# Performance work log

Hardware: AMD Instinct MI355X
Metric: run time of the kernel (lower is better)

The kernel has to match this reference:

```python
import jax, jax.numpy as jnp
import numpy as np

H = 16  # num_heads

def setup_inputs() -> dict:
    key = jax.random.key(0)
    ks = jax.random.split(key, 5)
    B, L, D = 2, 2048, 1024
    x = jax.random.normal(ks[0], (B, L, D), dtype=jnp.float32)
    # causal mask: masked_fill where mask == 0
    attn_mask = jnp.tril(jnp.ones((L, L), dtype=jnp.int32))
    scale = 1.0 / np.sqrt(D)
    Wq = jax.random.normal(ks[1], (D, D), dtype=jnp.float32) * scale
    Wk = jax.random.normal(ks[2], (D, D), dtype=jnp.float32) * scale
    Wv = jax.random.normal(ks[3], (D, D), dtype=jnp.float32) * scale
    Wo = jax.random.normal(ks[4], (D, D), dtype=jnp.float32) * scale
    return {"x": x, "attn_mask": attn_mask, "Wq": Wq, "Wk": Wk, "Wv": Wv, "Wo": Wo}

def reference(x, attn_mask, Wq, Wk, Wv, Wo):
    B, L, D = x.shape
    dh = D // H
    # nn.Linear with no bias: y = x @ W^T
    q = (x @ Wq.T).reshape(B, L, H, dh)
    k = (x @ Wk.T).reshape(B, L, H, dh)
    v = (x @ Wv.T).reshape(B, L, H, dh)
    # scores: [B, H, L, L]
    scores = jnp.einsum('blhd,bmhd->bhlm', q, k) / jnp.sqrt(jnp.array(dh, x.dtype))
    scores = jnp.where(attn_mask == 0, -jnp.inf, scores)
    attn = jax.nn.softmax(scores, axis=-1)
    out = jnp.einsum('bhlm,bmhd->blhd', attn, v).reshape(B, L, D)
    return out @ Wo.T
```

## Files before the change

kernel.cpp:

```cpp
#include <hip/hip_runtime.h>
#include <math.h>

#define L_SEQ  2048
#define D_MODEL 1024
#define N_HEAD 16
#define D_HEAD 64
#define B_SIZE 2

typedef __attribute__((ext_vector_type(8))) short bf16x8;
typedef __attribute__((ext_vector_type(4))) float f32x4;
typedef unsigned short u16;
typedef unsigned int u32;

__device__ __forceinline__ f32x4 mfma16(bf16x8 a, bf16x8 b, f32x4 c) {
    return __builtin_amdgcn_mfma_f32_16x16x32_bf16(a, b, c, 0, 0, 0);
}

__device__ __forceinline__ u16 f2bf(float x) {
    u32 u = __builtin_bit_cast(u32, x);
    u32 r = (u + 0x7FFFu + ((u >> 16) & 1u)) >> 16;
    return (u16)r;
}
__device__ __forceinline__ u16 f2bf_t(float x) {
    return (u16)(__builtin_bit_cast(u32, x) >> 16);
}
__device__ __forceinline__ float bf2f(u16 h) {
    u32 u = ((u32)h) << 16;
    return __builtin_bit_cast(float, u);
}

__device__ __forceinline__ void gl2lds16(const void* g, void* l) {
    __builtin_amdgcn_global_load_lds(
        (__attribute__((address_space(1))) void*)(g),
        (__attribute__((address_space(3))) void*)(l), 16, 0, 0);
}

__global__ __launch_bounds__(256) void split_hl(const float* __restrict__ in,
                                                u16* __restrict__ out) {
    const int idx = blockIdx.x * 256 + threadIdx.x;
    const int c4 = idx << 2;
    const int r = c4 >> 10, c = c4 & 1023;
    float4 v = *(const float4*)(in + c4);
    u16 h0 = f2bf(v.x), h1 = f2bf(v.y), h2 = f2bf(v.z), h3 = f2bf(v.w);
    ushort4 hi = make_ushort4(h0, h1, h2, h3);
    ushort4 lo = make_ushort4(f2bf(v.x - bf2f(h0)), f2bf(v.y - bf2f(h1)),
                              f2bf(v.z - bf2f(h2)), f2bf(v.w - bf2f(h3)));
    *(ushort4*)(out + (size_t)r * 2048 + c) = hi;
    *(ushort4*)(out + (size_t)r * 2048 + 1024 + c) = lo;
}

__global__ __launch_bounds__(256) void split_w4(
    const float* __restrict__ w0, const float* __restrict__ w1,
    const float* __restrict__ w2, const float* __restrict__ w3,
    u16* __restrict__ outbase) {
    const float* in = (blockIdx.y == 0) ? w0 : (blockIdx.y == 1) ? w1
                      : (blockIdx.y == 2) ? w2 : w3;
    u16* out = outbase + (size_t)blockIdx.y * 2097152;
    const int idx = blockIdx.x * 256 + threadIdx.x;
    const int c4 = idx << 2;
    const int r = c4 >> 10, c = c4 & 1023;
    float4 v = *(const float4*)(in + c4);
    u16 h0 = f2bf(v.x), h1 = f2bf(v.y), h2 = f2bf(v.z), h3 = f2bf(v.w);
    ushort4 hi = make_ushort4(h0, h1, h2, h3);
    ushort4 lo = make_ushort4(f2bf(v.x - bf2f(h0)), f2bf(v.y - bf2f(h1)),
                              f2bf(v.z - bf2f(h2)), f2bf(v.w - bf2f(h3)));
    *(ushort4*)(out + (size_t)r * 2048 + c) = hi;
    *(ushort4*)(out + (size_t)r * 2048 + 1024 + c) = lo;
}

__device__ __forceinline__ int kaOf(int x) {
    return (((x >> 4) == 1) ? 1024 : 0) + ((x << 6) & 1023);
}
__device__ __forceinline__ int kwOf(int x) {
    return (((x >> 4) == 0) ? 1024 : 0) + ((x << 6) & 1023);
}

#define SBAR()  do { __builtin_amdgcn_sched_barrier(0); \
                     __builtin_amdgcn_s_barrier(); \
                     __builtin_amdgcn_sched_barrier(0); } while (0)

__global__ __launch_bounds__(512) void gemm256_qkv(
    const u16* __restrict__ A2, const u16* __restrict__ Wall,
    u16* __restrict__ Qh, u16* __restrict__ Ql,
    u16* __restrict__ Kh, u16* __restrict__ Kl,
    u16* __restrict__ Vh) {
    extern __shared__ __align__(16) u16 smem[];

    const int t = threadIdx.x, l = t & 63, wid = t >> 6;
    const int id = blockIdx.x;
    const int wg = (id & 7) * 24 + (id >> 3);
    const int mt = wg / 12, ntile = wg % 12;
    const int m0 = mt << 8, n0 = ntile << 8;

    const int wrH = wid >> 2;
    const int wc = (wid & 3) << 6;
    const int bHalf = (wid & 3) >> 1;
    const int brB = (wid & 1) << 6;

    f32x4 acc[8][4];
#pragma unroll
    for (int i = 0; i < 8; ++i)
#pragma unroll
        for (int j = 0; j < 4; ++j) acc[i][j] = (f32x4){0.f, 0.f, 0.f, 0.f};

    const int sr = t >> 3, sc = t & 7;

    auto stageA = [&](int x, int half) {
        const int koff = kaOf(x);
        u16* dst = smem + ((x & 1) * 32768) + half * 8192;
        const u16* srcb = A2 + (size_t)(m0 + half * 128) * 2048 + koff;
#pragma unroll
        for (int p = 0; p < 2; ++p) {
            const int r = sr + p * 64;
            const int ck = sc ^ (r & 7);
            gl2lds16(srcb + (size_t)r * 2048 + ck * 8, dst + (t + p * 512) * 8);
        }
    };
    auto stageB = [&](int x, int half) {
        const int koff = kwOf(x);
        u16* dst = smem + 16384 + ((x & 1) * 32768) + half * 8192;
        const u16* srcb = Wall + (size_t)(n0 + half * 128) * 2048 + koff;
#pragma unroll
        for (int p = 0; p < 2; ++p) {
            const int r = sr + p * 64;
            const int ck = sc ^ (r & 7);
            gl2lds16(srcb + (size_t)r * 2048 + ck * 8, dst + (t + p * 512) * 8);
        }
    };
    auto dsA = [&](int s, int mh, int kc, bf16x8 af[4]) {
        const u16* Ab = smem + s * 32768 + wrH * 8192;
#pragma unroll
        for (int f = 0; f < 4; ++f) {
            const int r = mh * 64 + f * 16 + (l & 15);
            const int c8 = kc * 4 + (l >> 4);
            af[f] = *(const bf16x8*)&Ab[r * 64 + ((c8 ^ (r & 7)) << 3)];
        }
    };
    auto dsB = [&](int s, int kc, bf16x8 bfr[4]) {
        const u16* Bb = smem + 16384 + s * 32768 + bHalf * 8192;
#pragma unroll
        for (int f = 0; f < 4; ++f) {
            const int r = brB + f * 16 + (l & 15);
            const int c8 = kc * 4 + (l >> 4);
            bfr[f] = *(const bf16x8*)&Bb[r * 64 + ((c8 ^ (r & 7)) << 3)];
        }
    };

    stageB(0, 0); stageB(0, 1); stageA(0, 0); stageA(0, 1);
    stageB(1, 0); stageB(1, 1);
    __builtin_amdgcn_sched_barrier(0);
    asm volatile("s_waitcnt vmcnt(4)" ::: "memory");
    __builtin_amdgcn_s_barrier();
    __builtin_amdgcn_sched_barrier(0);

    const int NT = 48;
    bf16x8 breg0[4], breg1[4], af[4];
    for (int tt = 0; tt < NT; ++tt) {
        const int s = tt & 1;
        dsA(s, 0, 0, af); dsB(s, 0, breg0);
        if (tt + 1 < NT) stageA(tt + 1, 0);
        SBAR();
        __builtin_amdgcn_s_setprio(1);
#pragma unroll
        for (int f = 0; f < 4; ++f)
#pragma unroll
            for (int fn = 0; fn < 4; ++fn)
                acc[f][fn] = mfma16(af[f], breg0[fn], acc[f][fn]);
        __builtin_amdgcn_s_setprio(0);
        SBAR();
        dsA(s, 0, 1, af); dsB(s, 1, breg1);
        if (tt + 1 < NT) stageA(tt + 1, 1);
        SBAR();
        __builtin_amdgcn_s_setprio(1);
#pragma unroll
        for (int f = 0; f < 4; ++f)
#pragma unroll
            for (int fn = 0; fn < 4; ++fn)
                acc[f][fn] = mfma16(af[f], breg1[fn], acc[f][fn]);
        __builtin_amdgcn_s_setprio(0);
        SBAR();
        dsA(s, 1, 0, af);
        if (tt + 2 < NT) stageB(tt + 2, 0);
        SBAR();
        __builtin_amdgcn_s_setprio(1);
#pragma unroll
        for (int f = 0; f < 4; ++f)
#pragma unroll
            for (int fn = 0; fn < 4; ++fn)
                acc[4 + f][fn] = mfma16(af[f], breg0[fn], acc[4 + f][fn]);
        __builtin_amdgcn_s_setprio(0);
        SBAR();
        dsA(s, 1, 1, af);
        if (tt + 2 < NT) stageB(tt + 2, 1);
        SBAR();
        __builtin_amdgcn_s_setprio(1);
#pragma unroll
        for (int f = 0; f < 4; ++f)
#pragma unroll
            for (int fn = 0; fn < 4; ++fn)
                acc[4 + f][fn] = mfma16(af[f], breg1[fn], acc[4 + f][fn]);
        __builtin_amdgcn_s_setprio(0);
        __builtin_amdgcn_sched_barrier(0);
        if (tt + 2 < NT) {
            asm volatile("s_waitcnt vmcnt(4)" ::: "memory");
        } else if (tt + 1 < NT) {
            asm volatile("s_waitcnt vmcnt(0)" ::: "memory");
        }
        __builtin_amdgcn_s_barrier();
        __builtin_amdgcn_sched_barrier(0);
    }

#pragma unroll
    for (int fm = 0; fm < 8; ++fm)
#pragma unroll
        for (int fn = 0; fn < 4; ++fn)
#pragma unroll
            for (int rg = 0; rg < 4; ++rg) {
                const int gm = m0 + wrH * 128 + fm * 16 + ((l >> 4) << 2) + rg;
                const int gn = n0 + wc + fn * 16 + (l & 15);
                const int z = gn >> 10, col = gn & 1023;
                float v = acc[fm][fn][rg];
                if (z == 0) v *= 0.125f;
                const int b = gm >> 11, lq = gm & 2047;
                const int h = col >> 6, d = col & 63;
                const size_t oi = (((size_t)(b * 16 + h)) * 2048 + lq) * 64 + d;
                const u16 hi = f2bf(v);
                if (z == 0) { Qh[oi] = hi; Ql[oi] = f2bf(v - bf2f(hi)); }
                else if (z == 1) { Kh[oi] = hi; Kl[oi] = f2bf(v - bf2f(hi)); }
                else { Vh[oi] = hi; }
            }
}

template <int MODE>
__global__ __launch_bounds__(256) void gemm_ks(
    const u16* __restrict__ A2, const u16* __restrict__ Wbase,
    float* __restrict__ Cout) {
    __shared__ __align__(16) u16 As[128 * 32];
    __shared__ __align__(16) u16 Ws[128 * 32];
    const int t = threadIdx.x, l = t & 63, wid = t >> 6;
    const int m0 = blockIdx.y << 7, n0 = blockIdx.x << 7;
    const u16* W2 = Wbase;

    f32x4 acc[4][4];
#pragma unroll
    for (int i = 0; i < 4; ++i)
#pragma unroll
        for (int j = 0; j < 4; ++j) acc[i][j] = (f32x4){0.f, 0.f, 0.f, 0.f};

    int orow[2], ocs[2];
#pragma unroll
    for (int p = 0; p < 2; ++p) {
        int o = wid * 1024 + l * 16 + p * 4096;
        orow[p] = o >> 6;
        ocs[p] = ((o >> 4) & 3) ^ ((o >> 6) & 3);
    }
    const int wr = (wid >> 1) << 6, wc = (wid & 1) << 6;

    for (int k0 = 0; k0 < 3072; k0 += 32) {
        const int rg3 = k0 >> 10, kb = k0 & 1023;
        const int ka = (rg3 == 1 ? 1024 : 0) + kb;
        const int kw = (rg3 == 0 ? 1024 : 0) + kb;
        __syncthreads();
#pragma unroll
        for (int p = 0; p < 2; ++p) {
            gl2lds16(A2 + (size_t)(m0 + orow[p]) * 2048 + ka + ocs[p] * 8,
                     (u16*)As + (wid * 512 + p * 2048));
            gl2lds16(W2 + (size_t)(n0 + orow[p]) * 2048 + kw + ocs[p] * 8,
                     (u16*)Ws + (wid * 512 + p * 2048));
        }
        __syncthreads();
        bf16x8 af[4], bfr[4];
#pragma unroll
        for (int f = 0; f < 4; ++f) {
            int row = wr + (f << 4) + (l & 15);
            int ch = (l >> 4) ^ (row & 3);
            af[f] = *(const bf16x8*)&As[(row << 5) + (ch << 3)];
            int rown = wc + (f << 4) + (l & 15);
            int chn = (l >> 4) ^ (rown & 3);
            bfr[f] = *(const bf16x8*)&Ws[(rown << 5) + (chn << 3)];
        }
#pragma unroll
        for (int fm = 0; fm < 4; ++fm)
#pragma unroll
            for (int fn = 0; fn < 4; ++fn)
                acc[fm][fn] = mfma16(af[fm], bfr[fn], acc[fm][fn]);
    }

#pragma unroll
    for (int fm = 0; fm < 4; ++fm)
#pragma unroll
        for (int fn = 0; fn < 4; ++fn)
#pragma unroll
            for (int rg = 0; rg < 4; ++rg) {
                int gm = m0 + wr + (fm << 4) + ((l >> 4) << 2) + rg;
                int gn = n0 + wc + (fn << 4) + (l & 15);
                Cout[(size_t)gm * 1024 + gn] = acc[fm][fn][rg];
            }
}

__global__ __launch_bounds__(128) void vtrans(const u16* __restrict__ Vh,
                                              u16* __restrict__ Vth) {
    const int t = threadIdx.x;
    const int kt = (blockIdx.x << 1) + (t >> 6);
    const int h = blockIdx.y, b = blockIdx.z;
    const size_t base = ((size_t)(b * 16 + h)) * 131072;
    const int kv0 = kt << 6;
    const int st = t & 63;
    const int r0 = (st >> 3) << 3;
    const int c0 = (st & 7) << 3;
    ushort4 inv[8][2];
#pragma unroll
    for (int j = 0; j < 8; ++j) {
        const u16* p = Vh + base + (size_t)(kv0 + r0 + j) * 64 + c0;
        inv[j][0] = *(const ushort4*)p;
        inv[j][1] = *(const ushort4*)(p + 4);
    }
#pragma unroll
    for (int i = 0; i < 8; ++i) {
        u16 o[8];
#pragma unroll
        for (int j = 0; j < 8; ++j) {
            ushort4 vv = inv[j][i >> 2];
            const int ii = i & 3;
            o[j] = (ii == 0) ? vv.x : (ii == 1) ? vv.y : (ii == 2) ? vv.z : vv.w;
        }
        u16* q = Vth + base + (size_t)(c0 + i) * 2048 + kv0 + r0;
        *(ushort4*)q = make_ushort4(o[0], o[1], o[2], o[3]);
        *(ushort4*)(q + 4) = make_ushort4(o[4], o[5], o[6], o[7]);
    }
}

struct QTileState {
    bf16x8 qhf[2], qlf[2];
    f32x4 oacc[4];
    float mrow[4], lrow[4];
};

__device__ __forceinline__ void qstate_init(
    QTileState& st, const u16* Qh, const u16* Ql, size_t hb, int q0, int w, int l) {
    const int rowq = q0 + (w << 4) + (l & 15);
#pragma unroll
    for (int kc = 0; kc < 2; ++kc) {
        const size_t off = hb + (size_t)rowq * 64 + (((kc << 2) + (l >> 4)) << 3);
        st.qhf[kc] = *(const bf16x8*)(Qh + off);
        st.qlf[kc] = *(const bf16x8*)(Ql + off);
    }
#pragma unroll
    for (int i = 0; i < 4; ++i) {
        st.oacc[i] = (f32x4){0.f, 0.f, 0.f, 0.f};
        st.mrow[i] = -INFINITY;
        st.lrow[i] = 0.f;
    }
}

__device__ __forceinline__ void fa_compute(
    QTileState& st, const u16* bKh, const u16* bKl,
    const u16* bVh, int kv0, int q0, int w, int l, u16* Pw) {
    if (kv0 > q0 + (w << 4) + 15) return;

    f32x4 sacc[4];
#pragma unroll
    for (int nf = 0; nf < 4; ++nf) sacc[nf] = (f32x4){0.f, 0.f, 0.f, 0.f};
#pragma unroll
    for (int kc = 0; kc < 2; ++kc) {
        bf16x8 kh_[4], kl_[4];
#pragma unroll
        for (int nf = 0; nf < 4; ++nf) {
            const int row = (nf << 4) + (l & 15);
            const int ch = ((kc << 2) + (l >> 4)) ^ (row & 7);
            kh_[nf] = *(const bf16x8*)&bKh[(row << 6) + (ch << 3)];
            kl_[nf] = *(const bf16x8*)&bKl[(row << 6) + (ch << 3)];
        }
        __builtin_amdgcn_s_setprio(1);
#pragma unroll
        for (int nf = 0; nf < 4; ++nf) {
            sacc[nf] = mfma16(st.qhf[kc], kl_[nf], sacc[nf]);
            sacc[nf] = mfma16(st.qlf[kc], kh_[nf], sacc[nf]);
            sacc[nf] = mfma16(st.qhf[kc], kh_[nf], sacc[nf]);
        }
        __builtin_amdgcn_s_setprio(0);
    }

    const bool domask = (kv0 + 63) > (q0 + (w << 4));
    float pm[4] = {-INFINITY, -INFINITY, -INFINITY, -INFINITY};
    float sv[4][4];
#pragma unroll
    for (int nf = 0; nf < 4; ++nf)
#pragma unroll
        for (int rg = 0; rg < 4; ++rg) {
            float x = sacc[nf][rg];
            if (domask) {
                const int colg = kv0 + (nf << 4) + (l & 15);
                const int rowg = q0 + (w << 4) + ((l >> 4) << 2) + rg;
                if (colg > rowg) x = -INFINITY;
            }
            sv[nf][rg] = x;
            pm[rg] = fmaxf(pm[rg], x);
        }
#pragma unroll
    for (int rg = 0; rg < 4; ++rg) {
        float v = pm[rg];
        v = fmaxf(v, __shfl_xor(v, 1));
        v = fmaxf(v, __shfl_xor(v, 2));
        v = fmaxf(v, __shfl_xor(v, 4));
        v = fmaxf(v, __shfl_xor(v, 8));
        pm[rg] = v;
    }
    const float need = fmaxf(fmaxf(pm[0] - st.mrow[0], pm[1] - st.mrow[1]),
                             fmaxf(pm[2] - st.mrow[2], pm[3] - st.mrow[3]));
    if (__any(need > 8.0f)) {
#pragma unroll
        for (int rg = 0; rg < 4; ++rg) {
            const float mn = fmaxf(st.mrow[rg], pm[rg]);
            const float al = __expf(st.mrow[rg] - mn);
            st.mrow[rg] = mn;
            st.lrow[rg] *= al;
#pragma unroll
            for (int nf = 0; nf < 4; ++nf) st.oacc[nf][rg] *= al;
        }
    }
    float ps[4] = {0.f, 0.f, 0.f, 0.f};
    u16 pb[4][4];
#pragma unroll
    for (int nf = 0; nf < 4; ++nf)
#pragma unroll
        for (int rg = 0; rg < 4; ++rg) {
            const float p = __expf(sv[nf][rg] - st.mrow[rg]);
            ps[rg] += p;
            pb[nf][rg] = f2bf_t(p);
        }
#pragma unroll
    for (int rg = 0; rg < 4; ++rg) {
        float v = ps[rg];
        v += __shfl_xor(v, 1);
        v += __shfl_xor(v, 2);
        v += __shfl_xor(v, 4);
        v += __shfl_xor(v, 8);
        st.lrow[rg] += v;
    }

#pragma unroll
    for (int nf = 0; nf < 4; ++nf)
#pragma unroll
        for (int rg = 0; rg < 4; ++rg) {
            const int r = ((l >> 4) << 2) + rg;
            const int c = (nf << 4) + (l & 15);
            const int ch = (c >> 3) ^ (r & 7);
            Pw[(r << 6) + (ch << 3) + (c & 7)] = pb[nf][rg];
        }
#pragma unroll
    for (int kc = 0; kc < 2; ++kc) {
        const int r = l & 15;
        const int chp = ((kc << 2) + (l >> 4)) ^ (r & 7);
        const bf16x8 pa = *(const bf16x8*)&Pw[(r << 6) + (chp << 3)];
        bf16x8 vh_[4];
#pragma unroll
        for (int nf = 0; nf < 4; ++nf) {
            const int row = (nf << 4) + (l & 15);
            const int cv = ((kc << 2) + (l >> 4)) ^ (row & 7);
            vh_[nf] = *(const bf16x8*)&bVh[(row << 6) + (cv << 3)];
        }
        __builtin_amdgcn_s_setprio(1);
#pragma unroll
        for (int nf = 0; nf < 4; ++nf)
            st.oacc[nf] = mfma16(pa, vh_[nf], st.oacc[nf]);
        __builtin_amdgcn_s_setprio(0);
    }
}

__device__ __forceinline__ void fa_epilogue(
    QTileState& st, u16* A2, int g, int q0, int w, int l) {
    const int b = g >> 4, h = g & 15;
    float inv[4];
#pragma unroll
    for (int rg = 0; rg < 4; ++rg) inv[rg] = 1.0f / st.lrow[rg];
#pragma unroll
    for (int nf = 0; nf < 4; ++nf)
#pragma unroll
        for (int rg = 0; rg < 4; ++rg) {
            const int rowq = q0 + (w << 4) + ((l >> 4) << 2) + rg;
            const int m = (b << 11) + rowq;
            const int d = (nf << 4) + (l & 15);
            const float v = st.oacc[nf][rg] * inv[rg];
            const u16 hi = f2bf(v);
            const u16 lo = f2bf(v - bf2f(hi));
            const size_t rb = (size_t)m * 2048;
            A2[rb + h * 64 + d] = hi;
            A2[rb + 1024 + h * 64 + d] = lo;
        }
}

__global__ __launch_bounds__(512) void flash_mfma(
    const u16* __restrict__ Qh, const u16* __restrict__ Ql,
    const u16* __restrict__ Kh, const u16* __restrict__ Kl,
    const u16* __restrict__ Vth,
    u16* __restrict__ A2) {
    extern __shared__ __align__(16) u16 smem[];
    u16* const KhsA = smem;
    u16* const KlsA = smem + 4096;
    u16* const VhsA = smem + 8192;
    u16* const KhsB = smem + 12288;
    u16* const KlsB = smem + 16384;
    u16* const VhsB = smem + 20480;
    u16* const Ps   = smem + 24576;

    const int t = threadIdx.x, l = t & 63, w = t >> 6;
    const int id = blockIdx.x;
    const int nid = ((id & 7) << 5) + (id >> 3);
    const int g = nid >> 3;
    const int p = nid & 7;
    const int q0A = p << 7;
    const int q0B = (15 - p) << 7;
    const size_t hb = (size_t)g * 131072;

    QTileState stA, stB;
    qstate_init(stA, Qh, Ql, hb, q0A, w, l);
    qstate_init(stB, Qh, Ql, hb, q0B, w, l);

    const int row_s = t >> 3;
    const int cs_s = (t & 7) ^ (row_s & 7);

    auto stage = [&](u16* dKh, u16* dKl, u16* dVh, int kt_) {
        const int kv0s = kt_ << 6;
        const size_t koff = hb + (size_t)(kv0s + row_s) * 64 + cs_s * 8;
        gl2lds16(Kh + koff, dKh + t * 8);
        gl2lds16(Kl + koff, dKl + t * 8);
        const size_t voff = hb + (size_t)row_s * 2048 + kv0s + cs_s * 8;
        gl2lds16(Vth + voff, dVh + t * 8);
    };

    u16* const Pw = Ps + (w << 10);
    const int ntA = (p << 1) + 2;
    const int ntB = 32 - (p << 1);

    stage(KhsA, KlsA, VhsA, 0);
    __syncthreads();
    for (int kt = 0; kt < ntB; kt += 2) {
        stage(KhsB, KlsB, VhsB, kt + 1);
        fa_compute(stB, KhsA, KlsA, VhsA, kt << 6, q0B, w, l, Pw);
        if (kt < ntA)
            fa_compute(stA, KhsA, KlsA, VhsA, kt << 6, q0A, w, l, Pw);
        __syncthreads();
        if (kt + 2 < ntB) stage(KhsA, KlsA, VhsA, kt + 2);
        fa_compute(stB, KhsB, KlsB, VhsB, (kt + 1) << 6, q0B, w, l, Pw);
        if (kt + 1 < ntA)
            fa_compute(stA, KhsB, KlsB, VhsB, (kt + 1) << 6, q0A, w, l, Pw);
        __syncthreads();
    }

    fa_epilogue(stA, A2, g, q0A, w, l);
    fa_epilogue(stB, A2, g, q0B, w, l);
}

__global__ __launch_bounds__(256) void gemm_bt_f32(
    const float* __restrict__ A, const float* __restrict__ W,
    float* __restrict__ C, int M, int N, int K) {
    __shared__ float As[16][68];
    __shared__ float Bs[16][68];
    const int t = threadIdx.x;
    const int tx = t & 15, ty = t >> 4;
    const int m0 = blockIdx.y << 6, n0 = blockIdx.x << 6;
    const int lr = t >> 2, lc = (t & 3) << 2;
    const float* Ag = A + (size_t)(m0 + lr) * K + lc;
    const float* Wg = W + (size_t)(n0 + lr) * K + lc;
    float acc[4][4];
#pragma unroll
    for (int i = 0; i < 4; ++i)
#pragma unroll
        for (int j = 0; j < 4; ++j) acc[i][j] = 0.f;
    for (int k0 = 0; k0 < K; k0 += 16) {
        const float4 av = *(const float4*)(Ag + k0);
        const float4 wv = *(const float4*)(Wg + k0);
        __syncthreads();
        As[lc + 0][lr] = av.x; As[lc + 1][lr] = av.y;
        As[lc + 2][lr] = av.z; As[lc + 3][lr] = av.w;
        Bs[lc + 0][lr] = wv.x; Bs[lc + 1][lr] = wv.y;
        Bs[lc + 2][lr] = wv.z; Bs[lc + 3][lr] = wv.w;
        __syncthreads();
#pragma unroll
        for (int kk = 0; kk < 16; ++kk) {
            const float4 a = *(const float4*)&As[kk][ty << 2];
            const float4 b = *(const float4*)&Bs[kk][tx << 2];
            acc[0][0] += a.x * b.x; acc[0][1] += a.x * b.y; acc[0][2] += a.x * b.z; acc[0][3] += a.x * b.w;
            acc[1][0] += a.y * b.x; acc[1][1] += a.y * b.y; acc[1][2] += a.y * b.z; acc[1][3] += a.y * b.w;
            acc[2][0] += a.z * b.x; acc[2][1] += a.z * b.y; acc[2][2] += a.z * b.z; acc[2][3] += a.z * b.w;
            acc[3][0] += a.w * b.x; acc[3][1] += a.w * b.y; acc[3][2] += a.w * b.z; acc[3][3] += a.w * b.w;
        }
    }
#pragma unroll
    for (int i = 0; i < 4; ++i) {
        float4 o;
        o.x = acc[i][0]; o.y = acc[i][1]; o.z = acc[i][2]; o.w = acc[i][3];
        *(float4*)&C[(size_t)(m0 + (ty << 2) + i) * N + n0 + (tx << 2)] = o;
    }
}

#define SW(row, seg) ((((seg) ^ (((row) + ((row) >> 4)) & 15)) << 2))

__global__ __launch_bounds__(256) void flash_f32(
    const float* __restrict__ Q, const float* __restrict__ K,
    const float* __restrict__ V, float* __restrict__ O) {
    __shared__ float Qs[64 * 64];
    __shared__ float KPs[64 * 64];
    __shared__ float Vs[64 * 64];
    const int t = threadIdx.x;
    const int tx = t & 15, ty = t >> 4;
    const int qt = blockIdx.x, h = blockIdx.y, b = blockIdx.z;
    const int q0 = qt << 6;
    const size_t hbase = (size_t)b * L_SEQ * D_MODEL + (size_t)h * D_HEAD;
#pragma unroll
    for (int i = 0; i < 4; ++i) {
        const int idx = t + (i << 8);
        const int rr = idx >> 4, seg = idx & 15;
        const float4 qv = *(const float4*)&Q[hbase + (size_t)(q0 + rr) * D_MODEL + (seg << 2)];
        *(float4*)&Qs[rr * 64 + SW(rr, seg)] = qv;
    }
    float m[4], lr_[4], oacc[4][4];
#pragma unroll
    for (int i = 0; i < 4; ++i) {
        m[i] = -INFINITY; lr_[i] = 0.f;
#pragma unroll
        for (int j = 0; j < 4; ++j) oacc[i][j] = 0.f;
    }
    const int ntile = qt + 1;
    for (int kt = 0; kt < ntile; ++kt) {
        const int kv0 = kt << 6;
        __syncthreads();
#pragma unroll
        for (int i = 0; i < 4; ++i) {
            const int idx = t + (i << 8);
            const int rr = idx >> 4, seg = idx & 15;
            const float4 kv = *(const float4*)&K[hbase + (size_t)(kv0 + rr) * D_MODEL + (seg << 2)];
            const float4 vv = *(const float4*)&V[hbase + (size_t)(kv0 + rr) * D_MODEL + (seg << 2)];
            *(float4*)&KPs[rr * 64 + SW(rr, seg)] = kv;
            *(float4*)&Vs[rr * 64 + SW(rr, seg)] = vv;
        }
        __syncthreads();
        float s[4][4];
#pragma unroll
        for (int i = 0; i < 4; ++i)
#pragma unroll
            for (int j = 0; j < 4; ++j) s[i][j] = 0.f;
#pragma unroll
        for (int seg = 0; seg < 16; ++seg) {
            float4 qv[4], kv[4];
#pragma unroll
            for (int i = 0; i < 4; ++i) {
                const int R = (ty << 2) + i;
                qv[i] = *(const float4*)&Qs[R * 64 + SW(R, seg)];
            }
#pragma unroll
            for (int j = 0; j < 4; ++j) {
                const int Cc = (tx << 2) + j;
                kv[j] = *(const float4*)&KPs[Cc * 64 + SW(Cc, seg)];
            }
#pragma unroll
            for (int i = 0; i < 4; ++i)
#pragma unroll
                for (int j = 0; j < 4; ++j)
                    s[i][j] += qv[i].x * kv[j].x + qv[i].y * kv[j].y +
                               qv[i].z * kv[j].z + qv[i].w * kv[j].w;
        }
        const bool diag = (kt == qt);
        float tm[4];
#pragma unroll
        for (int i = 0; i < 4; ++i) {
            tm[i] = -INFINITY;
#pragma unroll
            for (int j = 0; j < 4; ++j) {
                float sval = s[i][j] * 0.125f;
                if (diag) {
                    const int Cg = kv0 + (tx << 2) + j;
                    const int Rg = q0 + (ty << 2) + i;
                    if (Cg > Rg) sval = -INFINITY;
                }
                s[i][j] = sval;
                tm[i] = fmaxf(tm[i], sval);
            }
            tm[i] = fmaxf(tm[i], __shfl_xor(tm[i], 1));
            tm[i] = fmaxf(tm[i], __shfl_xor(tm[i], 2));
            tm[i] = fmaxf(tm[i], __shfl_xor(tm[i], 4));
            tm[i] = fmaxf(tm[i], __shfl_xor(tm[i], 8));
        }
        float p[4][4];
#pragma unroll
        for (int i = 0; i < 4; ++i) {
            const float mn = fmaxf(m[i], tm[i]);
            const float alpha = __expf(m[i] - mn);
            m[i] = mn;
            float psum = 0.f;
#pragma unroll
            for (int j = 0; j < 4; ++j) {
                p[i][j] = __expf(s[i][j] - mn);
                psum += p[i][j];
            }
            psum += __shfl_xor(psum, 1);
            psum += __shfl_xor(psum, 2);
            psum += __shfl_xor(psum, 4);
            psum += __shfl_xor(psum, 8);
            lr_[i] = lr_[i] * alpha + psum;
#pragma unroll
            for (int j = 0; j < 4; ++j) oacc[i][j] *= alpha;
        }
        __syncthreads();
#pragma unroll
        for (int i = 0; i < 4; ++i) {
            const int R = (ty << 2) + i;
            float4 pv;
            pv.x = p[i][0]; pv.y = p[i][1]; pv.z = p[i][2]; pv.w = p[i][3];
            *(float4*)&KPs[R * 64 + SW(R, tx)] = pv;
        }
        __syncthreads();
#pragma unroll
        for (int cs = 0; cs < 16; ++cs) {
            float pc[4][4];
            float4 vr[4];
#pragma unroll
            for (int i = 0; i < 4; ++i) {
                const int R = (ty << 2) + i;
                const float4 pr = *(const float4*)&KPs[R * 64 + SW(R, cs)];
                pc[i][0] = pr.x; pc[i][1] = pr.y; pc[i][2] = pr.z; pc[i][3] = pr.w;
            }
#pragma unroll
            for (int cc = 0; cc < 4; ++cc) {
                const int Cr = (cs << 2) + cc;
                vr[cc] = *(const float4*)&Vs[Cr * 64 + SW(Cr, tx)];
            }
#pragma unroll
            for (int i = 0; i < 4; ++i)
#pragma unroll
                for (int cc = 0; cc < 4; ++cc) {
                    oacc[i][0] += pc[i][cc] * vr[cc].x;
                    oacc[i][1] += pc[i][cc] * vr[cc].y;
                    oacc[i][2] += pc[i][cc] * vr[cc].z;
                    oacc[i][3] += pc[i][cc] * vr[cc].w;
                }
        }
    }
#pragma unroll
    for (int i = 0; i < 4; ++i) {
        const int R = (ty << 2) + i;
        const float invl = 1.0f / lr_[i];
        float4 o;
        o.x = oacc[i][0] * invl; o.y = oacc[i][1] * invl;
        o.z = oacc[i][2] * invl; o.w = oacc[i][3] * invl;
        *(float4*)&O[hbase + (size_t)(q0 + R) * D_MODEL + (tx << 2)] = o;
    }
}

extern "C" void kernel_launch(void* const* d_in, const int* in_sizes, int n_in,
                              void* d_out, int out_size, void* d_ws, size_t ws_size,
                              hipStream_t stream) {
    const float* x  = (const float*)d_in[0];
    const float* Wq = (const float*)d_in[2];
    const float* Wk = (const float*)d_in[3];
    const float* Wv = (const float*)d_in[4];
    const float* Wo = (const float*)d_in[5];
    float* out = (float*)d_out;

    if (ws_size >= 83886080ull) {
        char* ws = (char*)d_ws;
        u16* x2  = (u16*)(ws);
        u16* Wq2 = (u16*)(ws + 16777216);
        u16* Wo2 = (u16*)(ws + 29360128);
        u16* Qh  = (u16*)(ws + 33554432);
        u16* Ql  = (u16*)(ws + 41943040);
        u16* Kh  = (u16*)(ws + 50331648);
        u16* Kl  = (u16*)(ws + 58720256);
        u16* Vth = (u16*)(ws + 67108864);
        u16* Vh  = (u16*)d_out;

        hipFuncSetAttribute((const void*)flash_mfma,
                            hipFuncAttributeMaxDynamicSharedMemorySize, 65536);
        hipFuncSetAttribute((const void*)gemm256_qkv,
                            hipFuncAttributeMaxDynamicSharedMemorySize, 131072);

        split_hl<<<4096, 256, 0, stream>>>(x, x2);
        split_w4<<<dim3(1024, 4), 256, 0, stream>>>(Wq, Wk, Wv, Wo, Wq2);
        gemm256_qkv<<<192, 512, 131072, stream>>>(x2, Wq2, Qh, Ql, Kh, Kl, Vh);
        vtrans<<<dim3(16, 16, 2), 128, 0, stream>>>(Vh, Vth);
        flash_mfma<<<256, 512, 65536, stream>>>(Qh, Ql, Kh, Kl, Vth, x2);
        gemm_ks<0><<<dim3(8, 32), 256, 0, stream>>>(x2, Wo2, out);
    } else {
        const int M = B_SIZE * L_SEQ, N = D_MODEL, Kd = D_MODEL;
        float* Qw = (float*)d_ws;
        float* Kw = Qw + (size_t)M * D_MODEL;
        float* Vw = Kw + (size_t)M * D_MODEL;
        float* Aw = Vw + (size_t)M * D_MODEL;
        dim3 gg(N / 64, M / 64);
        gemm_bt_f32<<<gg, 256, 0, stream>>>(x, Wq, Qw, M, N, Kd);
        gemm_bt_f32<<<gg, 256, 0, stream>>>(x, Wk, Kw, M, N, Kd);
        gemm_bt_f32<<<gg, 256, 0, stream>>>(x, Wv, Vw, M, N, Kd);
        flash_f32<<<dim3(L_SEQ / 64, N_HEAD, B_SIZE), 256, 0, stream>>>(Qw, Kw, Vw, Aw);
        gemm_bt_f32<<<gg, 256, 0, stream>>>(Aw, Wo, out, M, N, Kd);
    }
}
```

Baseline: 250.8 us.

## Interleave two query tiles per KV unit, retile output GEMM, merge split kernels

```diff
diff --git a/kernel.cpp b/kernel.cpp
--- a/kernel.cpp
+++ b/kernel.cpp
@@ -35,28 +35,24 @@
         (__attribute__((address_space(3))) void*)(l), 16, 0, 0);
 }
 
-__global__ __launch_bounds__(256) void split_hl(const float* __restrict__ in,
-                                                u16* __restrict__ out) {
-    const int idx = blockIdx.x * 256 + threadIdx.x;
-    const int c4 = idx << 2;
-    const int r = c4 >> 10, c = c4 & 1023;
-    float4 v = *(const float4*)(in + c4);
-    u16 h0 = f2bf(v.x), h1 = f2bf(v.y), h2 = f2bf(v.z), h3 = f2bf(v.w);
-    ushort4 hi = make_ushort4(h0, h1, h2, h3);
-    ushort4 lo = make_ushort4(f2bf(v.x - bf2f(h0)), f2bf(v.y - bf2f(h1)),
-                              f2bf(v.z - bf2f(h2)), f2bf(v.w - bf2f(h3)));
-    *(ushort4*)(out + (size_t)r * 2048 + c) = hi;
-    *(ushort4*)(out + (size_t)r * 2048 + 1024 + c) = lo;
-}
-
-__global__ __launch_bounds__(256) void split_w4(
+__global__ __launch_bounds__(256) void split_all(
+    const float* __restrict__ x,
     const float* __restrict__ w0, const float* __restrict__ w1,
     const float* __restrict__ w2, const float* __restrict__ w3,
-    u16* __restrict__ outbase) {
-    const float* in = (blockIdx.y == 0) ? w0 : (blockIdx.y == 1) ? w1
-                      : (blockIdx.y == 2) ? w2 : w3;
-    u16* out = outbase + (size_t)blockIdx.y * 2097152;
-    const int idx = blockIdx.x * 256 + threadIdx.x;
+    u16* __restrict__ x2, u16* __restrict__ wout) {
+    const int id = blockIdx.x;
+    const float* in;
+    u16* out;
+    int idx;
+    if (id < 4096) {
+        in = x; out = x2; idx = id * 256 + threadIdx.x;
+    } else {
+        const int wi = (id - 4096) >> 10;
+        const int blk = (id - 4096) & 1023;
+        in = (wi == 0) ? w0 : (wi == 1) ? w1 : (wi == 2) ? w2 : w3;
+        out = wout + (size_t)wi * 2097152;
+        idx = blk * 256 + threadIdx.x;
+    }
     const int c4 = idx << 2;
     const int r = c4 >> 10, c = c4 & 1023;
     float4 v = *(const float4*)(in + c4);
@@ -231,69 +227,71 @@
             }
 }
 
-template <int MODE>
-__global__ __launch_bounds__(256) void gemm_ks(
-    const u16* __restrict__ A2, const u16* __restrict__ Wbase,
+__global__ __launch_bounds__(256) void gemm_wo(
+    const u16* __restrict__ A2, const u16* __restrict__ W2,
     float* __restrict__ Cout) {
     __shared__ __align__(16) u16 As[128 * 32];
-    __shared__ __align__(16) u16 Ws[128 * 32];
+    __shared__ __align__(16) u16 Ws2[64 * 32];
     const int t = threadIdx.x, l = t & 63, wid = t >> 6;
-    const int m0 = blockIdx.y << 7, n0 = blockIdx.x << 7;
-    const u16* W2 = Wbase;
-
-    f32x4 acc[4][4];
+    const int id = blockIdx.x;
+    const int nid = ((id & 7) << 6) + (id >> 3);
+    const int m0 = (nid >> 4) << 7;
+    const int n0 = (nid & 15) << 6;
+    const int wm = wid >> 1, wn = wid & 1;
+
+    f32x4 acc[4][2];
 #pragma unroll
     for (int i = 0; i < 4; ++i)
 #pragma unroll
-        for (int j = 0; j < 4; ++j) acc[i][j] = (f32x4){0.f, 0.f, 0.f, 0.f};
-
-    int orow[2], ocs[2];
-#pragma unroll
-    for (int p = 0; p < 2; ++p) {
-        int o = wid * 1024 + l * 16 + p * 4096;
-        orow[p] = o >> 6;
-        ocs[p] = ((o >> 4) & 3) ^ ((o >> 6) & 3);
-    }
-    const int wr = (wid >> 1) << 6, wc = (wid & 1) << 6;
+        for (int j = 0; j < 2; ++j) acc[i][j] = (f32x4){0.f, 0.f, 0.f, 0.f};
+
+    const int arow0 = t >> 2, ach0 = (t & 3) ^ (arow0 & 3);
+    const int arow1 = (t + 256) >> 2, ach1 = (t & 3) ^ (arow1 & 3);
+    const int brow = t >> 2, bch = (t & 3) ^ (brow & 3);
 
     for (int k0 = 0; k0 < 3072; k0 += 32) {
         const int rg3 = k0 >> 10, kb = k0 & 1023;
         const int ka = (rg3 == 1 ? 1024 : 0) + kb;
         const int kw = (rg3 == 0 ? 1024 : 0) + kb;
         __syncthreads();
-#pragma unroll
-        for (int p = 0; p < 2; ++p) {
-            gl2lds16(A2 + (size_t)(m0 + orow[p]) * 2048 + ka + ocs[p] * 8,
-                     (u16*)As + (wid * 512 + p * 2048));
-            gl2lds16(W2 + (size_t)(n0 + orow[p]) * 2048 + kw + ocs[p] * 8,
-                     (u16*)Ws + (wid * 512 + p * 2048));
-        }
-        __syncthreads();
-        bf16x8 af[4], bfr[4];
+        gl2lds16(A2 + (size_t)(m0 + arow0) * 2048 + ka + ach0 * 8,
+                 (u16*)As + t * 8);
+        gl2lds16(A2 + (size_t)(m0 + arow1) * 2048 + ka + ach1 * 8,
+                 (u16*)As + (t + 256) * 8);
+        if (t < 256)
+            gl2lds16(W2 + (size_t)(n0 + brow) * 2048 + kw + bch * 8,
+                     (u16*)Ws2 + t * 8);
+        __syncthreads();
+        bf16x8 af[4], bfr[2];
 #pragma unroll
         for (int f = 0; f < 4; ++f) {
-            int row = wr + (f << 4) + (l & 15);
-            int ch = (l >> 4) ^ (row & 3);
+            const int row = wm * 64 + f * 16 + (l & 15);
+            const int ch = (l >> 4) ^ (row & 3);
             af[f] = *(const bf16x8*)&As[(row << 5) + (ch << 3)];
-            int rown = wc + (f << 4) + (l & 15);
-            int chn = (l >> 4) ^ (rown & 3);
-            bfr[f] = *(const bf16x8*)&Ws[(rown << 5) + (chn << 3)];
-        }
+        }
+#pragma unroll
+        for (int f = 0; f < 2; ++f) {
+            const int rown = wn * 32 + f * 16 + (l & 15);
+            const int chn = (l >> 4) ^ (rown & 3);
+            bfr[f] = *(const bf16x8*)&Ws2[(rown << 5) + (chn << 3)];
+        }
+        __builtin_amdgcn_s_setprio(1);
 #pragma unroll
         for (int fm = 0; fm < 4; ++fm)
 #pragma unroll
-            for (int fn = 0; fn < 4; ++fn)
+            for (int fn = 0; fn < 2; ++fn)
                 acc[fm][fn] = mfma16(af[fm], bfr[fn], acc[fm][fn]);
+        __builtin_amdgcn_s_setprio(0);
     }
 
 #pragma unroll
     for (int fm = 0; fm < 4; ++fm)
 #pragma unroll
-        for (int fn = 0; fn < 4; ++fn)
+        for (int fn = 0; fn < 2; ++fn)
 #pragma unroll
             for (int rg = 0; rg < 4; ++rg) {
-                int gm = m0 + wr + (fm << 4) + ((l >> 4) << 2) + rg;
-                int gn = n0 + wc + (fn << 4) + (l & 15);
+                const int gm = m0 + wm * 64 + fm * 16 + ((l >> 4) << 2) + rg;
+                const int gn = n0 + wn * 32 + fn * 16 + (l & 15);
                 Cout[(size_t)gm * 1024 + gn] = acc[fm][fn][rg];
             }
 }
@@ -353,11 +351,9 @@
     }
 }
 
-__device__ __forceinline__ void fa_compute(
+__device__ __forceinline__ void fa_qk_softmax(
     QTileState& st, const u16* bKh, const u16* bKl,
-    const u16* bVh, int kv0, int q0, int w, int l, u16* Pw) {
-    if (kv0 > q0 + (w << 4) + 15) return;
-
+    int kv0, int q0, int w, int l, u16 pb[4][4]) {
     f32x4 sacc[4];
 #pragma unroll
     for (int nf = 0; nf < 4; ++nf) sacc[nf] = (f32x4){0.f, 0.f, 0.f, 0.f};
@@ -420,7 +416,6 @@
         }
     }
     float ps[4] = {0.f, 0.f, 0.f, 0.f};
-    u16 pb[4][4];
 #pragma unroll
     for (int nf = 0; nf < 4; ++nf)
 #pragma unroll
@@ -438,7 +433,9 @@
         v += __shfl_xor(v, 8);
         st.lrow[rg] += v;
     }
-
+}
+
+__device__ __forceinline__ void fa_writeP(const u16 pb[4][4], int l, u16* Pw) {
 #pragma unroll
     for (int nf = 0; nf < 4; ++nf)
 #pragma unroll
@@ -448,24 +445,6 @@
             const int ch = (c >> 3) ^ (r & 7);
             Pw[(r << 6) + (ch << 3) + (c & 7)] = pb[nf][rg];
         }
-#pragma unroll
-    for (int kc = 0; kc < 2; ++kc) {
-        const int r = l & 15;
-        const int chp = ((kc << 2) + (l >> 4)) ^ (r & 7);
-        const bf16x8 pa = *(const bf16x8*)&Pw[(r << 6) + (chp << 3)];
-        bf16x8 vh_[4];
-#pragma unroll
-        for (int nf = 0; nf < 4; ++nf) {
-            const int row = (nf << 4) + (l & 15);
-            const int cv = ((kc << 2) + (l >> 4)) ^ (row & 7);
-            vh_[nf] = *(const bf16x8*)&bVh[(row << 6) + (cv << 3)];
-        }
-        __builtin_amdgcn_s_setprio(1);
-#pragma unroll
-        for (int nf = 0; nf < 4; ++nf)
-            st.oacc[nf] = mfma16(pa, vh_[nf], st.oacc[nf]);
-        __builtin_amdgcn_s_setprio(0);
-    }
 }
 
 __device__ __forceinline__ void fa_epilogue(
@@ -502,7 +481,8 @@
     u16* const KhsB = smem + 12288;
     u16* const KlsB = smem + 16384;
     u16* const VhsB = smem + 20480;
-    u16* const Ps   = smem + 24576;
+    u16* const PsB  = smem + 24576;
+    u16* const PsA  = smem + 32768;
 
     const int t = threadIdx.x, l = t & 63, w = t >> 6;
     const int id = blockIdx.x;
@@ -529,22 +509,57 @@
         gl2lds16(Vth + voff, dVh + t * 8);
     };
 
-    u16* const Pw = Ps + (w << 10);
+    u16* const PwB = PsB + (w << 10);
+    u16* const PwA = PsA + (w << 10);
     const int ntA = (p << 1) + 2;
     const int ntB = 32 - (p << 1);
+
+    auto unit = [&](const u16* bKh, const u16* bKl, const u16* bVh, int kt_) {
+        const int kv0 = kt_ << 6;
+        const bool aB = kv0 <= q0B + (w << 4) + 15;
+        const bool aA = (kt_ < ntA) && (kv0 <= q0A + (w << 4) + 15);
+        if (!aB && !aA) return;
+        u16 pbB[4][4], pbA[4][4];
+        if (aB) fa_qk_softmax(stB, bKh, bKl, kv0, q0B, w, l, pbB);
+        if (aA) fa_qk_softmax(stA, bKh, bKl, kv0, q0A, w, l, pbA);
+        if (aB) fa_writeP(pbB, l, PwB);
+        if (aA) fa_writeP(pbA, l, PwA);
+#pragma unroll
+        for (int kc = 0; kc < 2; ++kc) {
+            bf16x8 vh_[4];
+#pragma unroll
+            for (int nf = 0; nf < 4; ++nf) {
+                const int row = (nf << 4) + (l & 15);
+                const int cv = ((kc << 2) + (l >> 4)) ^ (row & 7);
+                vh_[nf] = *(const bf16x8*)&bVh[(row << 6) + (cv << 3)];
+            }
+            const int r = l & 15;
+            const int chp = ((kc << 2) + (l >> 4)) ^ (r & 7);
+            __builtin_amdgcn_s_setprio(1);
+            if (aB) {
+                const bf16x8 pa = *(const bf16x8*)&PwB[(r << 6) + (chp << 3)];
+#pragma unroll
+                for (int nf = 0; nf < 4; ++nf)
+                    stB.oacc[nf] = mfma16(pa, vh_[nf], stB.oacc[nf]);
+            }
+            if (aA) {
+                const bf16x8 pa = *(const bf16x8*)&PwA[(r << 6) + (chp << 3)];
+#pragma unroll
+                for (int nf = 0; nf < 4; ++nf)
+                    stA.oacc[nf] = mfma16(pa, vh_[nf], stA.oacc[nf]);
+            }
+            __builtin_amdgcn_s_setprio(0);
+        }
+    };
 
     stage(KhsA, KlsA, VhsA, 0);
     __syncthreads();
     for (int kt = 0; kt < ntB; kt += 2) {
         stage(KhsB, KlsB, VhsB, kt + 1);
-        fa_compute(stB, KhsA, KlsA, VhsA, kt << 6, q0B, w, l, Pw);
-        if (kt < ntA)
-            fa_compute(stA, KhsA, KlsA, VhsA, kt << 6, q0A, w, l, Pw);
+        unit(KhsA, KlsA, VhsA, kt);
         __syncthreads();
         if (kt + 2 < ntB) stage(KhsA, KlsA, VhsA, kt + 2);
-        fa_compute(stB, KhsB, KlsB, VhsB, (kt + 1) << 6, q0B, w, l, Pw);
-        if (kt + 1 < ntA)
-            fa_compute(stA, KhsB, KlsB, VhsB, (kt + 1) << 6, q0A, w, l, Pw);
+        unit(KhsB, KlsB, VhsB, kt + 1);
         __syncthreads();
     }
 
@@ -771,16 +786,15 @@
         u16* Vh  = (u16*)d_out;
 
         hipFuncSetAttribute((const void*)flash_mfma,
-                            hipFuncAttributeMaxDynamicSharedMemorySize, 65536);
+                            hipFuncAttributeMaxDynamicSharedMemorySize, 81920);
         hipFuncSetAttribute((const void*)gemm256_qkv,
                             hipFuncAttributeMaxDynamicSharedMemorySize, 131072);
 
-        split_hl<<<4096, 256, 0, stream>>>(x, x2);
-        split_w4<<<dim3(1024, 4), 256, 0, stream>>>(Wq, Wk, Wv, Wo, Wq2);
+        split_all<<<8192, 256, 0, stream>>>(x, Wq, Wk, Wv, Wo, x2, Wq2);
         gemm256_qkv<<<192, 512, 131072, stream>>>(x2, Wq2, Qh, Ql, Kh, Kl, Vh);
         vtrans<<<dim3(16, 16, 2), 128, 0, stream>>>(Vh, Vth);
-        flash_mfma<<<256, 512, 65536, stream>>>(Qh, Ql, Kh, Kl, Vth, x2);
-        gemm_ks<0><<<dim3(8, 32), 256, 0, stream>>>(x2, Wo2, out);
+        flash_mfma<<<256, 512, 81920, stream>>>(Qh, Ql, Kh, Kl, Vth, x2);
+        gemm_wo<<<512, 256, 0, stream>>>(x2, Wo2, out);
     } else {
         const int M = B_SIZE * L_SEQ, N = D_MODEL, Kd = D_MODEL;
         float* Qw = (float*)d_ws;
```

Result: faster. 244.8 us (-2.4%).
